# Performance work log

Measured on AMD Instinct MI355X. Metric: run time of the kernel, lower is better.

The kernel has to match this reference:

```python
import jax, jax.numpy as jnp
import numpy as np
from jax import lax

NUM_CLASS = 1000
LOW_DIM = 128
PROTO_M = 0.99
B_UPD = 1024
B_SIM = 65536
EPS = 1e-12  # F.normalize eps


def setup_inputs() -> dict:
    key = jax.random.key(0)
    k1, k2, k3, k4 = jax.random.split(key, 4)
    pred_feat = jax.random.normal(k1, (B_UPD, LOW_DIM), dtype=jnp.float32)
    pseudo_label = jax.random.randint(k2, (B_UPD,), 0, NUM_CLASS, dtype=jnp.int32)
    prototypes = jax.random.normal(k3, (NUM_CLASS, LOW_DIM), dtype=jnp.float32)
    feat = jax.random.normal(k4, (B_SIM, LOW_DIM), dtype=jnp.float32)
    return {"pred_feat": pred_feat, "pseudo_label": pseudo_label,
            "prototypes": prototypes, "feat": feat}


def _update_proto(prototypes, pred_feat, pseudo_label, m=PROTO_M):
    # Sequential per-sample EMA scatter (order matters when labels repeat),
    # expressed as a lax.scan recurrence over the batch.
    def step(protos, xl):
        f, lab = xl
        new = m * protos[lab] + (1.0 - m) * f
        return protos.at[lab].set(new), None
    prototypes, _ = lax.scan(step, prototypes, (pred_feat, pseudo_label))
    # F.normalize(p=2, dim=1): x / max(||x||_2, eps)
    norms = jnp.sqrt(jnp.sum(prototypes * prototypes, axis=1, keepdims=True))
    return prototypes / jnp.maximum(norms, EPS)


def reference(pred_feat, pseudo_label, prototypes, feat):
    protos = _update_proto(prototypes, pred_feat, pseudo_label)
    # cal_proto_sim: feat @ prototypes.T (prototypes detached in original)
    protos = lax.stop_gradient(protos)
    sim = jnp.matmul(feat, protos.T)  # [B_SIM, NUM_CLASS]
    return sim
```

## Files before the change

kernel.cpp:

```cpp
#include <hip/hip_runtime.h>
#include <hip/hip_bf16.h>
#include <cstdint>
#include <cstddef>

#define NUM_CLASS 1000
#define NPAD      1024
#define LOW_DIM   128
#define B_UPD     1024
#define B_SIM     65536

typedef short bf16x8 __attribute__((ext_vector_type(8)));
typedef float f32x4  __attribute__((ext_vector_type(4)));

__device__ __forceinline__ unsigned short f2bf(float f) {
  union { float f; unsigned u; } a; a.f = f;
  unsigned u = a.u;
  return (unsigned short)((u + 0x7fffu + ((u >> 16) & 1u)) >> 16);
}

__global__ void proto_update_kernel(const float* __restrict__ pred_feat,
                                    const int*   __restrict__ labels,
                                    const float* __restrict__ protos_in,
                                    unsigned short* __restrict__ protos_sw) {
  int c = blockIdx.x;
  int d = threadIdx.x;
  float p = 0.0f;
  if (c < NUM_CLASS) {
    p = protos_in[c * LOW_DIM + d];
    #pragma unroll 4
    for (int k = 0; k < B_UPD / 64; ++k) {
      int lab = labels[k * 64 + (d & 63)];
      unsigned long long m = __ballot(lab == c);
      while (m) {
        int b = __builtin_ctzll(m);
        m &= (m - 1);
        p = 0.99f * p + 0.01f * pred_feat[(size_t)(k * 64 + b) * LOW_DIM + d];
      }
    }
  }
  float sq = p * p;
  #pragma unroll
  for (int o = 1; o < 64; o <<= 1) sq += __shfl_xor(sq, o, 64);
  __shared__ float wsum[2];
  if ((d & 63) == 0) wsum[d >> 6] = sq;
  __syncthreads();
  float total = wsum[0] + wsum[1];
  unsigned short v = f2bf(p / fmaxf(sqrtf(total), 1e-12f));
  int g = c >> 4, r = c & 15, kk = d >> 5, j = (d >> 3) & 3, e = d & 7;
  protos_sw[(size_t)((g * 4 + kk) * 64 + j * 16 + r) * 8 + e] = v;
}

#define BM   32
#define TPB2 512
#define CPAD 132
#define EPW  (16 * CPAD)

__global__ __launch_bounds__(TPB2, 4)
void gemm_sim_kernel(const float* __restrict__ A,
                     const unsigned short* __restrict__ Bsw,
                     float* __restrict__ C) {
  __shared__ unsigned char smem[8 * EPW * 4];
  int t  = threadIdx.x;
  int m0 = blockIdx.x * BM;

  {
    int row = t >> 4, c8 = t & 15;
    const float4* s = reinterpret_cast<const float4*>(A + (size_t)(m0 + row) * LOW_DIM + c8 * 8);
    float4 v0 = s[0], v1 = s[1];
    uint4 q;
    q.x = f2bf(v0.x) | ((unsigned)f2bf(v0.y) << 16);
    q.y = f2bf(v0.z) | ((unsigned)f2bf(v0.w) << 16);
    q.z = f2bf(v1.x) | ((unsigned)f2bf(v1.y) << 16);
    q.w = f2bf(v1.z) | ((unsigned)f2bf(v1.w) << 16);
    *reinterpret_cast<uint4*>(smem + row * 256 + ((c8 * 16) ^ ((row & 7) << 4))) = q;
  }
  __syncthreads();

  int lane = t & 63;
  int w    = t >> 6;
  int lr   = lane & 15;
  int lkb  = (lane >> 4) * 16;

  f32x4 acc[2][8];
  #pragma unroll
  for (int m = 0; m < 2; ++m)
    #pragma unroll
    for (int n = 0; n < 8; ++n)
      acc[m][n] = (f32x4){0.f, 0.f, 0.f, 0.f};

  #pragma unroll
  for (int kk = 0; kk < 4; ++kk) {
    int kb = kk * 64 + lkb;
    bf16x8 af[2];
    #pragma unroll
    for (int m = 0; m < 2; ++m) {
      int row = m * 16 + lr;
      af[m] = *reinterpret_cast<const bf16x8*>(smem + row * 256 + (kb ^ ((row & 7) << 4)));
    }
    #pragma unroll
    for (int n = 0; n < 8; ++n) {
      int g = w * 8 + n;
      bf16x8 bf = *reinterpret_cast<const bf16x8*>(
          Bsw + ((size_t)(g * 4 + kk) * 64 + lane) * 8);
      #pragma unroll
      for (int m = 0; m < 2; ++m)
        acc[m][n] = __builtin_amdgcn_mfma_f32_16x16x32_bf16(af[m], bf, acc[m][n], 0, 0, 0);
    }
  }
  __syncthreads();

  float* myT = reinterpret_cast<float*>(smem) + w * EPW;
  #pragma unroll
  for (int m = 0; m < 2; ++m) {
    int rbase = (lane >> 4) * 4;
    #pragma unroll
    for (int n = 0; n < 8; ++n) {
      #pragma unroll
      for (int r = 0; r < 4; ++r)
        myT[(rbase + r) * CPAD + n * 16 + lr] = acc[m][n][r];
    }
    #pragma unroll
    for (int it = 0; it < 8; ++it) {
      int idx = it * 64 + lane;
      int row = idx >> 5, c4 = idx & 31;
      f32x4 v = *reinterpret_cast<const f32x4*>(myT + row * CPAD + c4 * 4);
      int col = w * 128 + c4 * 4;
      if (col < NUM_CLASS) {
        *reinterpret_cast<f32x4*>(C + (size_t)(m0 + m * 16 + row) * NUM_CLASS + col) = v;
      }
    }
  }
}

extern "C" void kernel_launch(void* const* d_in, const int* in_sizes, int n_in,
                              void* d_out, int out_size, void* d_ws, size_t ws_size,
                              hipStream_t stream) {
  const float* pred_feat = (const float*)d_in[0];
  const int*   labels    = (const int*)d_in[1];
  const float* protos    = (const float*)d_in[2];
  const float* feat      = (const float*)d_in[3];
  float* out = (float*)d_out;

  unsigned short* protos_sw = (unsigned short*)d_ws;

  proto_update_kernel<<<NPAD, 128, 0, stream>>>(pred_feat, labels, protos, protos_sw);
  gemm_sim_kernel<<<B_SIM / BM, TPB2, 0, stream>>>(feat, protos_sw, out);
}
```

Measured before the change: 74.02 us.

## Shrink GEMM block to 4 waves with 4 sub-tile passes and smaller LDS staging

```diff
diff --git a/kernel.cpp b/kernel.cpp
--- a/kernel.cpp
+++ b/kernel.cpp
@@ -50,21 +50,23 @@
   protos_sw[(size_t)((g * 4 + kk) * 64 + j * 16 + r) * 8 + e] = v;
 }
 
-#define BM   32
-#define TPB2 512
-#define CPAD 132
-#define EPW  (16 * CPAD)
+#define BM      32
+#define TPB2    256
+#define TSTRIDE 68
 
-__global__ __launch_bounds__(TPB2, 4)
+__global__ __launch_bounds__(TPB2, 5)
 void gemm_sim_kernel(const float* __restrict__ A,
                      const unsigned short* __restrict__ Bsw,
                      float* __restrict__ C) {
-  __shared__ unsigned char smem[8 * EPW * 4];
+  __shared__ alignas(16) unsigned char Als[BM * 256];
+  __shared__ alignas(16) float Tbuf[4][16 * TSTRIDE];
   int t  = threadIdx.x;
   int m0 = blockIdx.x * BM;
 
-  {
-    int row = t >> 4, c8 = t & 15;
+  #pragma unroll
+  for (int it = 0; it < 2; ++it) {
+    int idx = it * TPB2 + t;
+    int row = idx >> 4, c8 = idx & 15;
     const float4* s = reinterpret_cast<const float4*>(A + (size_t)(m0 + row) * LOW_DIM + c8 * 8);
     float4 v0 = s[0], v1 = s[1];
     uint4 q;
@@ -72,7 +74,7 @@
     q.y = f2bf(v0.z) | ((unsigned)f2bf(v0.w) << 16);
     q.z = f2bf(v1.x) | ((unsigned)f2bf(v1.y) << 16);
     q.w = f2bf(v1.z) | ((unsigned)f2bf(v1.w) << 16);
-    *reinterpret_cast<uint4*>(smem + row * 256 + ((c8 * 16) ^ ((row & 7) << 4))) = q;
+    *reinterpret_cast<uint4*>(Als + row * 256 + ((c8 * 16) ^ ((row & 7) << 4))) = q;
   }
   __syncthreads();
 
@@ -80,53 +82,56 @@
   int w    = t >> 6;
   int lr   = lane & 15;
   int lkb  = (lane >> 4) * 16;
-
-  f32x4 acc[2][8];
-  #pragma unroll
-  for (int m = 0; m < 2; ++m)
-    #pragma unroll
-    for (int n = 0; n < 8; ++n)
-      acc[m][n] = (f32x4){0.f, 0.f, 0.f, 0.f};
+  float* myT = Tbuf[w];
 
   #pragma unroll
-  for (int kk = 0; kk < 4; ++kk) {
-    int kb = kk * 64 + lkb;
-    bf16x8 af[2];
+  for (int s = 0; s < 4; ++s) {
+    int gbase = w * 16 + s * 4;
+    f32x4 acc[2][4];
+    #pragma unroll
+    for (int m = 0; m < 2; ++m)
+      #pragma unroll
+      for (int n = 0; n < 4; ++n)
+        acc[m][n] = (f32x4){0.f, 0.f, 0.f, 0.f};
+
+    #pragma unroll
+    for (int kk = 0; kk < 4; ++kk) {
+      int kb = kk * 64 + lkb;
+      bf16x8 af[2];
+      #pragma unroll
+      for (int m = 0; m < 2; ++m) {
+        int row = m * 16 + lr;
+        af[m] = *reinterpret_cast<const bf16x8*>(Als + row * 256 + (kb ^ ((row & 7) << 4)));
+      }
+      #pragma unroll
+      for (int n = 0; n < 4; ++n) {
+        bf16x8 bf = *reinterpret_cast<const bf16x8*>(
+            Bsw + ((size_t)((gbase + n) * 4 + kk) * 64 + lane) * 8);
+        #pragma unroll
+        for (int m = 0; m < 2; ++m)
+          acc[m][n] = __builtin_amdgcn_mfma_f32_16x16x32_bf16(af[m], bf, acc[m][n], 0, 0, 0);
+      }
+    }
+
+    int wc = gbase * 16;
     #pragma unroll
     for (int m = 0; m < 2; ++m) {
-      int row = m * 16 + lr;
-      af[m] = *reinterpret_cast<const bf16x8*>(smem + row * 256 + (kb ^ ((row & 7) << 4)));
-    }
-    #pragma unroll
-    for (int n = 0; n < 8; ++n) {
-      int g = w * 8 + n;
-      bf16x8 bf = *reinterpret_cast<const bf16x8*>(
-          Bsw + ((size_t)(g * 4 + kk) * 64 + lane) * 8);
+      int rbase = (lane >> 4) * 4;
       #pragma unroll
-      for (int m = 0; m < 2; ++m)
-        acc[m][n] = __builtin_amdgcn_mfma_f32_16x16x32_bf16(af[m], bf, acc[m][n], 0, 0, 0);
-    }
-  }
-  __syncthreads();
-
-  float* myT = reinterpret_cast<float*>(smem) + w * EPW;
-  #pragma unroll
-  for (int m = 0; m < 2; ++m) {
-    int rbase = (lane >> 4) * 4;
-    #pragma unroll
-    for (int n = 0; n < 8; ++n) {
+      for (int n = 0; n < 4; ++n)
+        #pragma unroll
+        for (int r = 0; r < 4; ++r)
+          myT[(rbase + r) * TSTRIDE + n * 16 + lr] = acc[m][n][r];
       #pragma unroll
-      for (int r = 0; r < 4; ++r)
-        myT[(rbase + r) * CPAD + n * 16 + lr] = acc[m][n][r];
-    }
-    #pragma unroll
-    for (int it = 0; it < 8; ++it) {
-      int idx = it * 64 + lane;
-      int row = idx >> 5, c4 = idx & 31;
-      f32x4 v = *reinterpret_cast<const f32x4*>(myT + row * CPAD + c4 * 4);
-      int col = w * 128 + c4 * 4;
-      if (col < NUM_CLASS) {
-        *reinterpret_cast<f32x4*>(C + (size_t)(m0 + m * 16 + row) * NUM_CLASS + col) = v;
+      for (int it = 0; it < 4; ++it) {
+        int idx = it * 64 + lane;
+        int row = idx >> 4;
+        int c4  = idx & 15;
+        f32x4 v = *reinterpret_cast<const f32x4*>(myT + row * TSTRIDE + c4 * 4);
+        int col = wc + c4 * 4;
+        if (col < NUM_CLASS) {
+          *reinterpret_cast<f32x4*>(C + (size_t)(m0 + m * 16 + row) * NUM_CLASS + col) = v;
+        }
       }
     }
   }
```

New measurement: 83.26 us. +12.5%, slower.

## Process four row tiles per GEMM block with prefetch of next A tile

Applied to the files above, without the earlier changes.

```diff
diff --git a/kernel.cpp b/kernel.cpp
--- a/kernel.cpp
+++ b/kernel.cpp
@@ -50,84 +50,113 @@
   protos_sw[(size_t)((g * 4 + kk) * 64 + j * 16 + r) * 8 + e] = v;
 }
 
-#define BM   32
-#define TPB2 512
-#define CPAD 132
-#define EPW  (16 * CPAD)
+#define BM    32
+#define TILES 4
+#define TPB2  512
+#define CPAD  132
+#define EPW   (16 * CPAD)
 
 __global__ __launch_bounds__(TPB2, 4)
 void gemm_sim_kernel(const float* __restrict__ A,
                      const unsigned short* __restrict__ Bsw,
                      float* __restrict__ C) {
-  __shared__ unsigned char smem[8 * EPW * 4];
-  int t  = threadIdx.x;
-  int m0 = blockIdx.x * BM;
+  __shared__ unsigned char smem[8192 + 8 * EPW * 4];
+  int t    = threadIdx.x;
+  int lane = t & 63;
+  int w    = t >> 6;
+  int lr   = lane & 15;
+  int lkb  = (lane >> 4) * 16;
+  int arow = t >> 4, ac8 = t & 15;
+  float* myT = reinterpret_cast<float*>(smem + 8192) + w * EPW;
 
   {
-    int row = t >> 4, c8 = t & 15;
-    const float4* s = reinterpret_cast<const float4*>(A + (size_t)(m0 + row) * LOW_DIM + c8 * 8);
+    int m0 = blockIdx.x * (TILES * BM);
+    const float4* s = reinterpret_cast<const float4*>(A + (size_t)(m0 + arow) * LOW_DIM + ac8 * 8);
     float4 v0 = s[0], v1 = s[1];
     uint4 q;
     q.x = f2bf(v0.x) | ((unsigned)f2bf(v0.y) << 16);
     q.y = f2bf(v0.z) | ((unsigned)f2bf(v0.w) << 16);
     q.z = f2bf(v1.x) | ((unsigned)f2bf(v1.y) << 16);
     q.w = f2bf(v1.z) | ((unsigned)f2bf(v1.w) << 16);
-    *reinterpret_cast<uint4*>(smem + row * 256 + ((c8 * 16) ^ ((row & 7) << 4))) = q;
+    *reinterpret_cast<uint4*>(smem + arow * 256 + ((ac8 * 16) ^ ((arow & 7) << 4))) = q;
   }
   __syncthreads();
 
-  int lane = t & 63;
-  int w    = t >> 6;
-  int lr   = lane & 15;
-  int lkb  = (lane >> 4) * 16;
+  for (int tile = 0; tile < TILES; ++tile) {
+    int m0 = blockIdx.x * (TILES * BM) + tile * BM;
 
-  f32x4 acc[2][8];
-  #pragma unroll
-  for (int m = 0; m < 2; ++m)
+    f32x4 acc[2][8];
     #pragma unroll
-    for (int n = 0; n < 8; ++n)
-      acc[m][n] = (f32x4){0.f, 0.f, 0.f, 0.f};
+    for (int m = 0; m < 2; ++m)
+      #pragma unroll
+      for (int n = 0; n < 8; ++n)
+        acc[m][n] = (f32x4){0.f, 0.f, 0.f, 0.f};
 
-  #pragma unroll
-  for (int kk = 0; kk < 4; ++kk) {
-    int kb = kk * 64 + lkb;
-    bf16x8 af[2];
+    #pragma unroll
+    for (int kk = 0; kk < 4; ++kk) {
+      int kb = kk * 64 + lkb;
+      bf16x8 af[2];
+      #pragma unroll
+      for (int m = 0; m < 2; ++m) {
+        int row = m * 16 + lr;
+        af[m] = *reinterpret_cast<const bf16x8*>(smem + row * 256 + (kb ^ ((row & 7) << 4)));
+      }
+      #pragma unroll
+      for (int n = 0; n < 8; ++n) {
+        int g = w * 8 + n;
+        bf16x8 bf = *reinterpret_cast<const bf16x8*>(
+            Bsw + ((size_t)(g * 4 + kk) * 64 + lane) * 8);
+        #pragma unroll
+        for (int m = 0; m < 2; ++m)
+          acc[m][n] = __builtin_amdgcn_mfma_f32_16x16x32_bf16(af[m], bf, acc[m][n], 0, 0, 0);
+      }
+    }
+
+    float4 nv0, nv1;
+    bool have_next = (tile + 1 < TILES);
+    if (have_next) {
+      const float4* s = reinterpret_cast<const float4*>(
+          A + (size_t)(m0 + BM + arow) * LOW_DIM + ac8 * 8);
+      nv0 = s[0]; nv1 = s[1];
+    }
+
     #pragma unroll
     for (int m = 0; m < 2; ++m) {
-      int row = m * 16 + lr;
-      af[m] = *reinterpret_cast<const bf16x8*>(smem + row * 256 + (kb ^ ((row & 7) << 4)));
+      int rbase = (lane >> 4) * 4;
+      #pragma unroll
+      for (int n = 0; n < 8; ++n) {
+        #pragma unroll
+        for (int r = 0; r < 4; ++r)
+          myT[(rbase + r) * CPAD + n * 16 + lr] = acc[m][n][r];
+      }
+      #pragma unroll
+      for (int it = 0; it < 8; ++it) {
+        int idx = it * 64 + lane;
+        int row = idx >> 5, c4 = idx & 31;
+        f32x4 v = *reinterpret_cast<const f32x4*>(myT + row * CPAD + c4 * 4);
+        int col = w * 128 + c4 * 4;
+        if (col < NUM_CLASS) {
+          *reinterpret_cast<f32x4*>(C + (size_t)(m0 + m * 16 + row) * NUM_CLASS + col) = v;
+        }
+      }
     }
-    #pragma unroll
-    for (int n = 0; n < 8; ++n) {
-      int g = w * 8 + n;
-      bf16x8 bf = *reinterpret_cast<const bf16x8*>(
-          Bsw + ((size_t)(g * 4 + kk) * 64 + lane) * 8);
-      #pragma unroll
-      for (int m = 0; m < 2; ++m)
-        acc[m][n] = __builtin_amdgcn_mfma_f32_16x16x32_bf16(af[m], bf, acc[m][n], 0, 0, 0);
-    }
-  }
-  __syncthreads();
 
-  float* myT = reinterpret_cast<float*>(smem) + w * EPW;
-  #pragma unroll
-  for (int m = 0; m < 2; ++m) {
-    int rbase = (lane >> 4) * 4;
-    #pragma unroll
-    for (int n = 0; n < 8; ++n) {
-      #pragma unroll
-      for (int r = 0; r < 4; ++r)
-        myT[(rbase + r) * CPAD + n * 16 + lr] = acc[m][n][r];
-    }
-    #pragma unroll
-    for (int it = 0; it < 8; ++it) {
-      int idx = it * 64 + lane;
-      int row = idx >> 5, c4 = idx & 31;
-      f32x4 v = *reinterpret_cast<const f32x4*>(myT + row * CPAD + c4 * 4);
-      int col = w * 128 + c4 * 4;
-      if (col < NUM_CLASS) {
-        *reinterpret_cast<f32x4*>(C + (size_t)(m0 + m * 16 + row) * NUM_CLASS + col) = v;
-      }
+    if (have_next) {
+      __builtin_amdgcn_sched_barrier(0);
+      __builtin_amdgcn_s_barrier();
+      __builtin_amdgcn_sched_barrier(0);
+
+      uint4 q;
+      q.x = f2bf(nv0.x) | ((unsigned)f2bf(nv0.y) << 16);
+      q.y = f2bf(nv0.z) | ((unsigned)f2bf(nv0.w) << 16);
+      q.z = f2bf(nv1.x) | ((unsigned)f2bf(nv1.y) << 16);
+      q.w = f2bf(nv1.z) | ((unsigned)f2bf(nv1.w) << 16);
+      *reinterpret_cast<uint4*>(smem + arow * 256 + ((ac8 * 16) ^ ((arow & 7) << 4))) = q;
+
+      asm volatile("s_waitcnt lgkmcnt(0)" ::: "memory");
+      __builtin_amdgcn_sched_barrier(0);
+      __builtin_amdgcn_s_barrier();
+      __builtin_amdgcn_sched_barrier(0);
     }
   }
 }
@@ -144,5 +173,5 @@
   unsigned short* protos_sw = (unsigned short*)d_ws;
 
   proto_update_kernel<<<NPAD, 128, 0, stream>>>(pred_feat, labels, protos, protos_sw);
-  gemm_sim_kernel<<<B_SIM / BM, TPB2, 0, stream>>>(feat, protos_sw, out);
+  gemm_sim_kernel<<<B_SIM / (BM * TILES), TPB2, 0, stream>>>(feat, protos_sw, out);
 }
```

Result: slower. 242.3 us (+227.4%).
